# Kernel tuning notes

Measured on AMD Instinct MI355X. Metric: run time of the kernel, lower is better.

Reference implementation:

```python
import jax, jax.numpy as jnp
import numpy as np

D = 512      # model dim
NH = 8       # heads
DH = 64      # dim per head
M = 256      # num landmarks
ITERS = 6    # pinv iterations
EPS = 1e-5   # layernorm eps


def layer_norm(x, g, b):
    mu = x.mean(-1, keepdims=True)
    var = ((x - mu) ** 2).mean(-1, keepdims=True)
    return (x - mu) * jax.lax.rsqrt(var + EPS) * g + b


def moore_penrose_pinv(x, iters=ITERS):
    abs_x = jnp.abs(x)
    col = abs_x.sum(-1)
    row = abs_x.sum(-2)
    z = jnp.swapaxes(x, -1, -2) / (jnp.max(col) * jnp.max(row))
    I = jnp.eye(x.shape[-1], dtype=x.dtype)
    for _ in range(iters):
        xz = x @ z
        z = 0.25 * z @ (13 * I - xz @ (15 * I - xz @ (7 * I - xz)))
    return z


def nystrom_attention(x, w_qkv, w_out, b_out, res_w):
    B, n0, _ = x.shape
    pad = (M - n0 % M) % M
    x = jnp.pad(x, ((0, 0), (pad, 0), (0, 0)))  # pad at front, like lucidrains
    n = n0 + pad
    qkv = x @ w_qkv  # (B, n, 3*D), no bias
    q, k, v = jnp.split(qkv, 3, axis=-1)
    rs = lambda t: t.reshape(B, n, NH, DH).transpose(0, 2, 1, 3)  # (B,H,n,d)
    q = rs(q) * (DH ** -0.5)
    k = rs(k)
    v = rs(v)
    l = n // M
    q_l = q.reshape(B, NH, M, l, DH).mean(3)  # (B,H,M,d) landmark means
    k_l = k.reshape(B, NH, M, l, DH).mean(3)
    s1 = jnp.einsum('bhnd,bhmd->bhnm', q, k_l)
    s2 = jnp.einsum('bhmd,bhld->bhml', q_l, k_l)
    s3 = jnp.einsum('bhmd,bhnd->bhmn', q_l, k)
    a1 = jax.nn.softmax(s1, -1)
    a2 = jax.nn.softmax(s2, -1)
    a3 = jax.nn.softmax(s3, -1)
    out = a1 @ (moore_penrose_pinv(a2) @ (a3 @ v))  # (B,H,n,d)
    # depthwise residual conv over sequence: Conv2d(heads, heads, (33,1), groups=heads)
    res = jax.lax.conv_general_dilated(v, res_w, (1, 1), 'SAME',
                                       feature_group_count=NH,
                                       dimension_numbers=('NCHW', 'OIHW', 'NCHW'))
    out = out + res
    out = out.transpose(0, 2, 1, 3).reshape(B, n, NH * DH) @ w_out + b_out
    return out[:, -n0:]


def dwconv(x, w, b):
    y = jax.lax.conv_general_dilated(x, w, (1, 1), 'SAME',
                                     feature_group_count=x.shape[1],
                                     dimension_numbers=('NCHW', 'OIHW', 'NCHW'))
    return y + b[None, :, None, None]


def ppeg(x, pw7, pb7, pw5, pb5, pw3, pb3, Hh, Ww):
    cls, feat = x[:, :1], x[:, 1:]
    B, _, C = x.shape
    cnn = feat.transpose(0, 2, 1).reshape(B, C, Hh, Ww)
    y = cnn + dwconv(cnn, pw7, pb7) + dwconv(cnn, pw5, pb5) + dwconv(cnn, pw3, pb3)
    y = y.reshape(B, C, Hh * Ww).transpose(0, 2, 1)
    return jnp.concatenate([cls, y], axis=1)


def _forward(x, w_fc1, b_fc1, cls_token, ln1_g, ln1_b, qkv1_w, out1_w, out1_b, res1_w,
             ln2_g, ln2_b, qkv2_w, out2_w, out2_b, res2_w,
             pw7, pb7, pw5, pb5, pw3, pb3, lnf_g, lnf_b, w_fc2, b_fc2):
    h = jax.nn.relu(x @ w_fc1 + b_fc1)  # (B, N, 512)
    Hn = h.shape[1]
    s = int(np.ceil(np.sqrt(Hn)))  # static grid side
    add = s * s - Hn
    h = jnp.concatenate([h, h[:, :add]], axis=1)
    B = h.shape[0]
    cls = jnp.broadcast_to(cls_token, (B, 1, D))
    h = jnp.concatenate([cls, h], axis=1)
    h = h + nystrom_attention(layer_norm(h, ln1_g, ln1_b), qkv1_w, out1_w, out1_b, res1_w)
    h = ppeg(h, pw7, pb7, pw5, pb5, pw3, pb3, s, s)
    h = h + nystrom_attention(layer_norm(h, ln2_g, ln2_b), qkv2_w, out2_w, out2_b, res2_w)
    h = layer_norm(h, lnf_g, lnf_b)[:, 0]
    return h @ w_fc2 + b_fc2


def setup_inputs() -> dict:
    key = jax.random.key(0)
    ks = jax.random.split(key, 16)
    g = lambda k, shp, s=0.02: jax.random.normal(k, shp, dtype=jnp.float32) * s
    z = lambda n: jnp.zeros((n,), jnp.float32)
    o = lambda n: jnp.ones((n,), jnp.float32)
    B, N, DIN, NC = 2, 10000, 1024, 2
    return {
        'x': jax.random.normal(ks[0], (B, N, DIN), dtype=jnp.float32),
        'w_fc1': g(ks[1], (DIN, D)), 'b_fc1': z(D),
        'cls_token': g(ks[2], (1, 1, D), 1.0),
        'ln1_g': o(D), 'ln1_b': z(D),
        'qkv1_w': g(ks[3], (D, 3 * D)),
        'out1_w': g(ks[4], (D, D)), 'out1_b': z(D),
        'res1_w': g(ks[5], (NH, 1, 33, 1)),
        'ln2_g': o(D), 'ln2_b': z(D),
        'qkv2_w': g(ks[6], (D, 3 * D)),
        'out2_w': g(ks[7], (D, D)), 'out2_b': z(D),
        'res2_w': g(ks[8], (NH, 1, 33, 1)),
        'pw7': g(ks[9], (D, 1, 7, 7)), 'pb7': z(D),
        'pw5': g(ks[10], (D, 1, 5, 5)), 'pb5': z(D),
        'pw3': g(ks[11], (D, 1, 3, 3)), 'pb3': z(D),
        'lnf_g': o(D), 'lnf_b': z(D),
        'w_fc2': g(ks[12], (D, NC)), 'b_fc2': z(NC),
    }


def reference(x, w_fc1, b_fc1, cls_token, ln1_g, ln1_b, qkv1_w, out1_w, out1_b, res1_w,
              ln2_g, ln2_b, qkv2_w, out2_w, out2_b, res2_w,
              pw7, pb7, pw5, pb5, pw3, pb3, lnf_g, lnf_b, w_fc2, b_fc2):
    logits = _forward(x, w_fc1, b_fc1, cls_token, ln1_g, ln1_b, qkv1_w, out1_w, out1_b, res1_w,
                      ln2_g, ln2_b, qkv2_w, out2_w, out2_b, res2_w,
                      pw7, pb7, pw5, pb5, pw3, pb3, lnf_g, lnf_b, w_fc2, b_fc2)
    Y_prob = jax.nn.softmax(logits, -1)
    Y_hat = jnp.argmax(logits, -1)
    return logits, Y_prob, Y_hat
```

## Files before the change

### kernel.cpp

```cpp
#include <hip/hip_runtime.h>
#include <math.h>

#define FLAG_RELU 1
#define FLAG_BIAS 2
#define FLAG_ACC  4
#define FLAG_ATOMIC 8

static constexpr int BB   = 2;
static constexpr int N0   = 10000;
static constexpr int DIN  = 1024;
static constexpr int D    = 512;
static constexpr int NH   = 8;
static constexpr int DH   = 64;
static constexpr int MM   = 256;
static constexpr int SEQ  = 10240;
static constexpr int PADR = 239;
static constexpr int NTOK = 10001;
static constexpr int LL   = 40;
static constexpr float EPS_ = 1e-5f;

typedef short short8v __attribute__((ext_vector_type(8)));
typedef float f32x4 __attribute__((ext_vector_type(4)));

__device__ __forceinline__ void atomicMaxPosF(float* addr, float v) {
// ... 83 lines not shown
            size_t gb = (size_t)(n0 + srow) * ldbt + k0 + 32 + scg;
            pb0 = *(const uint4*)(BtH + gb); pb1 = *(const uint4*)(BtH + gb + 8);
            pb2 = *(const uint4*)(BtL + gb); pb3 = *(const uint4*)(BtL + gb + 8);
        }
        short8v ah[4], al[4];
        #pragma unroll
        for (int mi = 0; mi < 4; mi++) {
            int row = wm*64 + mi*16 + r;
            ah[mi] = *(const short8v*)&AsH[q*1024 + row*8];
            al[mi] = *(const short8v*)&AsL[q*1024 + row*8];
        }
        #pragma unroll
        for (int ni = 0; ni < 4; ni++) {
            int col = wn*64 + ni*16 + r;
            short8v bh = *(const short8v*)&BsH[q*1024 + col*8];
            short8v bl = *(const short8v*)&BsL[q*1024 + col*8];
            #pragma unroll
            for (int mi = 0; mi < 4; mi++) {
                acc[mi][ni] = __builtin_amdgcn_mfma_f32_16x16x32_bf16(ah[mi], bh, acc[mi][ni], 0,0,0);
                acc[mi][ni] = __builtin_amdgcn_mfma_f32_16x16x32_bf16(ah[mi], bl, acc[mi][ni], 0,0,0);
                acc[mi][ni] = __builtin_amdgcn_mfma_f32_16x16x32_bf16(al[mi], bh, acc[mi][ni], 0,0,0);
            }
        }
        __syncthreads();
    }
    #pragma unroll
    for (int mi = 0; mi < 4; mi++)
        #pragma unroll
        for (int ni = 0; ni < 4; ni++) {
            int gcol = n0 + wn*64 + ni*16 + r;
            float qs = (gcol < qcols) ? qscale : 1.f;
            float bv = (flags & FLAG_BIAS) ? bias[gcol] : 0.f;
            #pragma unroll
            for (int rg = 0; rg < 4; rg++) {
                int grow = m0 + wm*64 + mi*16 + q*4 + rg;
                if (grow >= M) continue;
                float v = acc[mi][ni][rg] * qs + bv;
                if (flags & FLAG_RELU) v = fmaxf(v, 0.f);
                float* cp = C + (size_t)grow * ldc + gcol;
                if (flags & FLAG_ACC) v += *cp;
                *cp = v;
            }
        }
}

__global__ __launch_bounds__(256)
void mbgemm64(const float* __restrict__ Abase, long long sAb, long long sAh, long long sAz, int lda,
              const ushort* __restrict__ BtH, const ushort* __restrict__ BtL,
              const float* __restrict__ Bnt, long long sBb, long long sBh, int ldb,
              float* __restrict__ Cbase, long long sCb, long long sCh, long long sCz, int ldc,
              ushort* __restrict__ eTH, ushort* __restrict__ eTL, long long sT, int ldct,
              const float* __restrict__ rowM, const float* __restrict__ rowI,
              int M, int N, int K, int nchunk,
              float dg, float bsc, float osc, int slab0, int flags)
{
    __shared__ ushort AsH[4*64*8], AsL[4*64*8], BsH[4*64*8], BsL[4*64*8];
    int zi = blockIdx.z / nchunk, ch = blockIdx.z % nchunk;
    int g = slab0 + zi, b = g >> 3, h = g & 7;
    const float* A = Abase + (size_t)b*sAb + (size_t)h*sAh + (size_t)zi*sAz;
    float* C = Cbase ? (Cbase + (size_t)b*sCb + (size_t)h*sCh + (size_t)zi*sCz) : nullptr;
    int kpc = K / nchunk;
    int kb = ch * kpc, ke = kb + kpc;
    int t = threadIdx.x;
    int m0 = blockIdx.y * 64, n0 = blockIdx.x * 64;
    int w = t >> 6, lane = t & 63, q = lane >> 4, r = lane & 15;
    int wm = w >> 1, wn = w & 1;
    f32x4 acc[2][2];
    #pragma unroll
    for (int i = 0; i < 2; i++)
        #pragma unroll
        for (int j = 0; j < 2; j++) acc[i][j] = (f32x4){0.f,0.f,0.f,0.f};

    int srow = t >> 2, scg = (t & 3) * 8;
    int qg = t & 3;
    float rmv = 0.f, riv = 1.f;
    bool doexp = (rowM != nullptr);
    if (doexp) {
        rmv = rowM[(size_t)zi * MM + m0 + srow];
        riv = rowI[(size_t)zi * MM + m0 + srow];
    }
    const float* Abp = Bnt ? (Bnt + (size_t)b*sBb + (size_t)h*sBh) : nullptr;
    float4 pa0, pa1;
    float4 pf0, pf1;
    uint4  pu0, pu1;
    {
        const float* ap = A + (size_t)(m0 + srow) * lda + kb + scg;
        pa0 = *(const float4*)ap; pa1 = *(const float4*)(ap+4);
        if (Bnt) {
            const float* bp = Abp + (size_t)(n0 + srow) * ldb + kb + scg;
            pf0 = *(const float4*)bp; pf1 = *(const float4*)(bp+4);
        } else {
            size_t gb = (size_t)b*sBb + (size_t)h*sBh + (size_t)(n0 + srow) * ldb + kb + scg;
            pu0 = *(const uint4*)(BtH + gb); pu1 = *(const uint4*)(BtL + gb);
        }
    }
    for (int k0 = kb; k0 < ke; k0 += 32) {
        {
            float4 qa0 = pa0, qa1 = pa1;
            if (doexp) {
                qa0.x = expf(qa0.x - rmv) * riv; qa0.y = expf(qa0.y - rmv) * riv;
                qa0.z = expf(qa0.z - rmv) * riv; qa0.w = expf(qa0.w - rmv) * riv;
                qa1.x = expf(qa1.x - rmv) * riv; qa1.y = expf(qa1.y - rmv) * riv;
                qa1.z = expf(qa1.z - rmv) * riv; qa1.w = expf(qa1.w - rmv) * riv;
            }
            ushort hb[8], lb[8];
            split4(qa0, &hb[0], &lb[0]);
            split4(qa1, &hb[4], &lb[4]);
            *(uint4*)&AsH[qg*512 + srow*8] = *(uint4*)&hb[0];
            *(uint4*)&AsL[qg*512 + srow*8] = *(uint4*)&lb[0];
            if (Bnt) {
                ushort hc[8], lc[8];
                split4(pf0, &hc[0], &lc[0]);
                split4(pf1, &hc[4], &lc[4]);
                *(uint4*)&BsH[qg*512 + srow*8] = *(uint4*)&hc[0];
                *(uint4*)&BsL[qg*512 + srow*8] = *(uint4*)&lc[0];
            } else {
                *(uint4*)&BsH[qg*512 + srow*8] = pu0;
                *(uint4*)&BsL[qg*512 + srow*8] = pu1;
            }
        }
        __syncthreads();
        if (k0 + 32 < ke) {
            const float* ap = A + (size_t)(m0 + srow) * lda + k0 + 32 + scg;
            pa0 = *(const float4*)ap; pa1 = *(const float4*)(ap+4);
            if (Bnt) {
                const float* bp = Abp + (size_t)(n0 + srow) * ldb + k0 + 32 + scg;
                pf0 = *(const float4*)bp; pf1 = *(const float4*)(bp+4);
            } else {
                size_t gb = (size_t)b*sBb + (size_t)h*sBh + (size_t)(n0 + srow) * ldb + k0 + 32 + scg;
                pu0 = *(const uint4*)(BtH + gb); pu1 = *(const uint4*)(BtL + gb);
            }
        }
        short8v ah[2], al[2];
        #pragma unroll
        for (int mi = 0; mi < 2; mi++) {
            int row = wm*32 + mi*16 + r;
            ah[mi] = *(const short8v*)&AsH[q*512 + row*8];
            al[mi] = *(const short8v*)&AsL[q*512 + row*8];
        }
        #pragma unroll
        for (int ni = 0; ni < 2; ni++) {
            int col = wn*32 + ni*16 + r;
            short8v bh = *(const short8v*)&BsH[q*512 + col*8];
            short8v bl = *(const short8v*)&BsL[q*512 + col*8];
            #pragma unroll
            for (int mi = 0; mi < 2; mi++) {
                acc[mi][ni] = __builtin_amdgcn_mfma_f32_16x16x32_bf16(ah[mi], bh, acc[mi][ni], 0,0,0);
                acc[mi][ni] = __builtin_amdgcn_mfma_f32_16x16x32_bf16(ah[mi], bl, acc[mi][ni], 0,0,0);
                acc[mi][ni] = __builtin_amdgcn_mfma_f32_16x16x32_bf16(al[mi], bh, acc[mi][ni], 0,0,0);
            }
        }
        __syncthreads();
    }
    bool dgnz = (dg != 0.f);
    #pragma unroll
    for (int mi = 0; mi < 2; mi++)
        #pragma unroll
        for (int ni = 0; ni < 2; ni++) {
            int gm0 = m0 + wm*32 + mi*16 + q*4;
            int gn  = n0 + wn*32 + ni*16 + r;
            float v[4];
            #pragma unroll
            for (int rg = 0; rg < 4; rg++) {
                float u = bsc * acc[mi][ni][rg];
                if (dgnz) u += dg * A[(size_t)(gm0+rg) * lda + gn];
                v[rg] = osc * u;
            }
            if (C) {
                if (flags & FLAG_ATOMIC) {
                    #pragma unroll
                    for (int rg = 0; rg < 4; rg++)
                        atomicAdd(C + (size_t)(gm0+rg) * ldc + gn, v[rg]);
                } else {
                    #pragma unroll
                    for (int rg = 0; rg < 4; rg++)
                        C[(size_t)(gm0+rg) * ldc + gn] = v[rg];
                }
            }
            if (eTH) {
                ushort4 hv, lv;
                hv.x = f2bf(v[0]); lv.x = f2bf(v[0] - bf2f(hv.x));
                hv.y = f2bf(v[1]); lv.y = f2bf(v[1] - bf2f(hv.y));
                hv.z = f2bf(v[2]); lv.z = f2bf(v[2] - bf2f(hv.z));
                hv.w = f2bf(v[3]); lv.w = f2bf(v[3] - bf2f(hv.w));
                size_t to = (size_t)g * sT + (size_t)gn * ldct + gm0;
                *(ushort4*)(eTH + to) = hv;
                *(ushort4*)(eTL + to) = lv;
            }
        }
}

__global__ __launch_bounds__(256)
void a1_fused(const float* __restrict__ qkv,
              const ushort* __restrict__ klH, const ushort* __restrict__ klL,
              const ushort* __restrict__ wbH, const ushort* __restrict__ wbL,
              float* __restrict__ attn)
{
    constexpr int LP = 264;
    __shared__ ushort PcH[32*LP], PcL[32*LP];
    __shared__ float redm[4][32];
    __shared__ float reds[4][32];
    int g = blockIdx.y, b = g >> 3, h = g & 7;
    int tok0 = blockIdx.x * 32;
    int t = threadIdx.x;
    int w = t >> 6, lane = t & 63, q = lane >> 4, r = lane & 15;

    f32x4 acc[2][4];
    #pragma unroll
    for (int i = 0; i < 2; i++)
        #pragma unroll
        for (int j = 0; j < 4; j++) acc[i][j] = (f32x4){0.f,0.f,0.f,0.f};
    #pragma unroll
    for (int k0 = 0; k0 < 64; k0 += 32) {
        short8v ah[2], al[2];
        #pragma unroll
        for (int mi = 0; mi < 2; mi++) {
            const float* ap = qkv + ((size_t)b*SEQ + tok0 + mi*16 + r) * 1536
                            + h*DH + k0 + q*8;
            split8r(ap, ah[mi], al[mi]);
        }
        #pragma unroll
        for (int ni = 0; ni < 4; ni++) {
            size_t kb = ((size_t)g*MM + w*64 + ni*16 + r) * DH + k0 + q*8;
            short8v bh = *(const short8v*)(klH + kb);
            short8v bl = *(const short8v*)(klL + kb);
            #pragma unroll
            for (int mi = 0; mi < 2; mi++) {
                acc[mi][ni] = __builtin_amdgcn_mfma_f32_16x16x32_bf16(ah[mi], bh, acc[mi][ni], 0,0,0);
                acc[mi][ni] = __builtin_amdgcn_mfma_f32_16x16x32_bf16(ah[mi], bl, acc[mi][ni], 0,0,0);
                acc[mi][ni] = __builtin_amdgcn_mfma_f32_16x16x32_bf16(al[mi], bh, acc[mi][ni], 0,0,0);
            }
        }
    }
    #pragma unroll
    for (int mi = 0; mi < 2; mi++)
        #pragma unroll
        for (int rg = 0; rg < 4; rg++) {
            float m = fmaxf(fmaxf(acc[mi][0][rg], acc[mi][1][rg]),
                            fmaxf(acc[mi][2][rg], acc[mi][3][rg]));
            for (int o = 8; o > 0; o >>= 1) m = fmaxf(m, __shfl_xor(m, o));
            if (r == 0) redm[w][mi*16 + q*4 + rg] = m;
        }
    __syncthreads();
    #pragma unroll
    for (int mi = 0; mi < 2; mi++)
        #pragma unroll
        for (int rg = 0; rg < 4; rg++) {
            int row = mi*16 + q*4 + rg;
            float gm = fmaxf(fmaxf(redm[0][row], redm[1][row]),
                             fmaxf(redm[2][row], redm[3][row]));
            float s = 0.f;
            #pragma unroll
            for (int ni = 0; ni < 4; ni++) {
                float e = expf(acc[mi][ni][rg] - gm);
                acc[mi][ni][rg] = e;
                s += e;
                int col = w*64 + ni*16 + r;
                ushort hv = f2bf(e);
                PcH[row*LP + col] = hv;
                PcL[row*LP + col] = f2bf(e - bf2f(hv));
            }
            for (int o = 8; o > 0; o >>= 1) s += __shfl_xor(s, o);
            if (r == 0) reds[w][row] = s;
        }
    __syncthreads();
    int wm = w & 1, wn = w >> 1;
    int prow = wm*16 + r;
    f32x4 oacc[2];
    #pragma unroll
    for (int ni = 0; ni < 2; ni++) oacc[ni] = (f32x4){0.f,0.f,0.f,0.f};
    #pragma unroll
    for (int k0 = 0; k0 < 8; k0++) {
        short8v ph = *(const short8v*)&PcH[prow*LP + k0*32 + q*8];
        short8v pl = *(const short8v*)&PcL[prow*LP + k0*32 + q*8];
        #pragma unroll
        for (int ni = 0; ni < 2; ni++) {
            size_t wo = ((size_t)g*64 + wn*32 + ni*16 + r) * MM + k0*32 + q*8;
            short8v bh = *(const short8v*)(wbH + wo);
            short8v bl = *(const short8v*)(wbL + wo);
            oacc[ni] = __builtin_amdgcn_mfma_f32_16x16x32_bf16(ph, bh, oacc[ni], 0,0,0);
            oacc[ni] = __builtin_amdgcn_mfma_f32_16x16x32_bf16(ph, bl, oacc[ni], 0,0,0);
            oacc[ni] = __builtin_amdgcn_mfma_f32_16x16x32_bf16(pl, bh, oacc[ni], 0,0,0);
        }
    }
    float inv[4];
    #pragma unroll
    for (int rg = 0; rg < 4; rg++) {
        int row = wm*16 + q*4 + rg;
        inv[rg] = 1.0f / (reds[0][row] + reds[1][row] + reds[2][row] + reds[3][row]);
    }
    #pragma unroll
    for (int ni = 0; ni < 2; ni++)
        #pragma unroll
        for (int rg = 0; rg < 4; rg++) {
            int tok = tok0 + wm*16 + q*4 + rg;
            attn[((size_t)b*SEQ + tok) * D + h*DH + wn*32 + ni*16 + r] = oacc[ni][rg] * inv[rg];
        }
}

__global__ __launch_bounds__(256)
void convsplitT(const float* __restrict__ in, ushort* __restrict__ oh, ushort* __restrict__ ol,
                int R, int C, int ldin, long long sInB, long long sInH, long long sInZ,
                int ldo, long long sOutZ)
{
    __shared__ float tile[32][33];
    int z = blockIdx.z, b = z >> 3, h = z & 7;
    const float* I = in + (size_t)b*sInB + (size_t)h*sInH + (size_t)z*sInZ;
    int p0 = blockIdx.x * 32, c0 = blockIdx.y * 32;
    int tx = threadIdx.x & 31, ty = threadIdx.x >> 5;
    #pragma unroll
    for (int k = 0; k < 4; k++) {
        int rr = p0 + ty + k*8, cc = c0 + tx;
        tile[ty + k*8][tx] = (rr < R && cc < C) ? I[(size_t)rr * ldin + cc] : 0.f;
    }
    __syncthreads();
    #pragma unroll
    for (int k = 0; k < 4; k++) {
        int rr = p0 + tx, cc = c0 + ty + k*8;
        if (rr < R && cc < C) {
            float f = tile[tx][ty + k*8];
            ushort hv = f2bf(f);
            size_t o = (size_t)z * sOutZ + (size_t)cc * ldo + rr;
            oh[o] = hv; ol[o] = f2bf(f - bf2f(hv));
        }
    }
}

__global__ void fill_cls(const float* __restrict__ cls, float* __restrict__ H) {
    H[(size_t)blockIdx.x * NTOK * D + threadIdx.x] = cls[threadIdx.x];
}

__global__ __launch_bounds__(256)
void ln_pad(const float* __restrict__ H, const float* __restrict__ g,
            const float* __restrict__ bt, float* __restrict__ out)
{
    int blk = blockIdx.x;
    int b = blk / SEQ, i = blk % SEQ;
    int t = threadIdx.x;
    float* orow = out + (size_t)blk * D;
    if (i < PADR) { orow[t] = 0.f; orow[t+256] = 0.f; return; }
    const float* x = H + ((size_t)b * NTOK + (i - PADR)) * D;
    float v0 = x[t], v1 = x[t+256];
    __shared__ float w1[4], w2[4];
    float s = v0 + v1;
    for (int o = 32; o > 0; o >>= 1) s += __shfl_xor(s, o);
    if ((t & 63) == 0) w1[t >> 6] = s;
    __syncthreads();
    float mu = (w1[0]+w1[1]+w1[2]+w1[3]) * (1.0f / D);
    float d0 = v0 - mu, d1 = v1 - mu;
    float qq = d0*d0 + d1*d1;
    for (int o = 32; o > 0; o >>= 1) qq += __shfl_xor(qq, o);
    if ((t & 63) == 0) w2[t >> 6] = qq;
    __syncthreads();
    float rs = rsqrtf((w2[0]+w2[1]+w2[2]+w2[3]) * (1.0f / D) + EPS_);
    orow[t]     = d0 * rs * g[t]     + bt[t];
    orow[t+256] = d1 * rs * g[t+256] + bt[t+256];
}

__global__ __launch_bounds__(512)
void landmarks(const float* __restrict__ qkv, float* __restrict__ ql,
               float* __restrict__ klt, ushort* __restrict__ klH, ushort* __restrict__ klL)
{
    int blk = blockIdx.x;
    int b = blk >> 8, m = blk & 255;
    int c = threadIdx.x;
    const float* base = qkv + ((size_t)b * SEQ + (size_t)m * LL) * 1536;
    float sq0=0,sq1=0,sq2=0,sq3=0, sk0=0,sk1=0,sk2=0,sk3=0;
    for (int tt = 0; tt < LL; tt += 4) {
        const float* rr = base + (size_t)tt * 1536;
        sq0 += rr[c];          sk0 += rr[512 + c];
        sq1 += rr[1536 + c];   sk1 += rr[1536 + 512 + c];
        sq2 += rr[3072 + c];   sk2 += rr[3072 + 512 + c];
        sq3 += rr[4608 + c];   sk3 += rr[4608 + 512 + c];
    }
    float sq = (sq0+sq1+sq2+sq3) * (1.0f / LL);
    float sk = (sk0+sk1+sk2+sk3) * (1.0f / LL);
    int h = c >> 6, d = c & 63;
    int slab = b * NH + h;
    ql [((size_t)slab * MM + m) * DH + d] = sq;
    klt[((size_t)slab * DH + d) * MM + m] = sk;
    size_t kidx = ((size_t)slab * MM + m) * DH + d;
    ushort kh = f2bf(sk);
    klH[kidx] = kh; klL[kidx] = f2bf(sk - bf2f(kh));
}

__global__ __launch_bounds__(256)
void s2_softmax(const float* __restrict__ ql, const float* __restrict__ klt,
                float* __restrict__ a2)
{
    int blk = blockIdx.x;
    int m = blk & 255, slab = blk >> 8;
    int j = threadIdx.x;
    __shared__ float q[64];
    __shared__ float red[256];
    if (j < 64) q[j] = ql[((size_t)slab * MM + m) * DH + j];
    __syncthreads();
    const float* kt = klt + (size_t)slab * DH * MM;
    float s = 0.f;
    #pragma unroll 8
    for (int kk = 0; kk < 64; kk++) s = fmaf(q[kk], kt[kk*MM + j], s);
    red[j] = s; __syncthreads();
    for (int o = 128; o > 0; o >>= 1) { if (j < o) red[j] = fmaxf(red[j], red[j+o]); __syncthreads(); }
    float mx = red[0]; __syncthreads();
    float e = expf(s - mx);
    red[j] = e; __syncthreads();
    for (int o = 128; o > 0; o >>= 1) { if (j < o) red[j] += red[j+o]; __syncthreads(); }
    a2[((size_t)slab * MM + m) * MM + j] = e / red[0];
}

__global__ void zero_scr(float* s) { if (threadIdx.x < 2) s[threadIdx.x] = 0.f; }

__global__ __launch_bounds__(256)
void a2_alpha(const float* __restrict__ a2, float* __restrict__ scr)
{
    int slab = blockIdx.x, t = threadIdx.x;
    const float* A = a2 + (size_t)slab * MM * MM;
    float cs = 0.f, rs = 0.f;
    for (int rr = 0; rr < MM; rr++) cs += fabsf(A[(size_t)rr * MM + t]);
    for (int cc = 0; cc < MM; cc++) rs += fabsf(A[(size_t)t * MM + cc]);
    __shared__ float red[256];
    red[t] = rs; __syncthreads();
    for (int o = 128; o > 0; o >>= 1) { if (t < o) red[t] = fmaxf(red[t], red[t+o]); __syncthreads(); }
    float mrs = red[0]; __syncthreads();
    red[t] = cs; __syncthreads();
    for (int o = 128; o > 0; o >>= 1) { if (t < o) red[t] = fmaxf(red[t], red[t+o]); __syncthreads(); }
    float mcs = red[0];
    if (t == 0) { atomicMaxPosF(scr + 0, mrs); atomicMaxPosF(scr + 1, mcs); }
}

__global__ __launch_bounds__(256)
void z_init(const float* __restrict__ a2, const float* __restrict__ scr,
            float* __restrict__ z, ushort* __restrict__ zTh, ushort* __restrict__ zTl)
{
    size_t idx = (size_t)blockIdx.x * 256 + threadIdx.x;
    int slab = (int)(idx >> 16), rr = (int)((idx >> 8) & 255), cc = (int)(idx & 255);
    float inv = 1.0f / (scr[0] * scr[1]);
    z[idx] = a2[((size_t)slab << 16) + (size_t)cc * MM + rr] * inv;
    float tv = a2[idx] * inv;
    ushort th = f2bf(tv);
    zTh[idx] = th; zTl[idx] = f2bf(tv - bf2f(th));
}

__global__ __launch_bounds__(256)
void s3_maxsum(const float* __restrict__ s3, float* __restrict__ rowM,
               float* __restrict__ rowI)
{
    const float* row = s3 + (size_t)blockIdx.x * SEQ;
    int t = threadIdx.x;
    float4 v[10];
    #pragma unroll
    for (int i = 0; i < 10; i++) v[i] = *(const float4*)(row + 4*(i*256 + t));
    float mx = -3.4e38f;
    #pragma unroll
    for (int i = 0; i < 10; i++)
        mx = fmaxf(mx, fmaxf(fmaxf(v[i].x, v[i].y), fmaxf(v[i].z, v[i].w)));
    __shared__ float red[4];
    for (int o = 32; o > 0; o >>= 1) mx = fmaxf(mx, __shfl_xor(mx, o));
    if ((t & 63) == 0) red[t >> 6] = mx;
    __syncthreads();
    mx = fmaxf(fmaxf(red[0], red[1]), fmaxf(red[2], red[3]));
    float sum = 0.f;
    #pragma unroll
    for (int i = 0; i < 10; i++) {
        sum += expf(v[i].x - mx) + expf(v[i].y - mx)
             + expf(v[i].z - mx) + expf(v[i].w - mx);
    }
    __shared__ float red2[4];
    for (int o = 32; o > 0; o >>= 1) sum += __shfl_xor(sum, o);
    if ((t & 63) == 0) red2[t >> 6] = sum;
    __syncthreads();
    if (t == 0) {
        rowM[blockIdx.x] = mx;
        rowI[blockIdx.x] = 1.0f / (red2[0] + red2[1] + red2[2] + red2[3]);
    }
}

__global__ __launch_bounds__(512)
void res_add(const float* __restrict__ qkv, const float* __restrict__ rw,
             float* __restrict__ attn)
{
    int blk = blockIdx.x;
    int b = blk / (SEQ/16), i0 = (blk % (SEQ/16)) * 16;
    int c = threadIdx.x, h = c >> 6;
    __shared__ float w[NH*33];
    if (c < NH*33) w[c] = rw[c];
    __syncthreads();
    float acc[16];
    float* ab = attn + ((size_t)b * SEQ + i0) * D + c;
    #pragma unroll
    for (int rr = 0; rr < 16; rr++) acc[rr] = ab[(size_t)rr * D];
    const float* vb = qkv + (size_t)b * SEQ * 1536 + 2*D + c;
    const float* wh = w + h * 33;
    #pragma unroll 4
    for (int jj = 0; jj < 48; jj++) {
        int j = i0 + jj - 16;
        float val = ((unsigned)j < (unsigned)SEQ) ? vb[(size_t)j * 1536] : 0.f;
        #pragma unroll
        for (int rr = 0; rr < 16; rr++) {
            int ky = jj - rr;
            if (ky >= 0 && ky < 33) acc[rr] = fmaf(val, wh[ky], acc[rr]);
        }
    }
    #pragma unroll
    for (int rr = 0; rr < 16; rr++) ab[(size_t)rr * D] = acc[rr];
}

__global__ __launch_bounds__(256)
void t_fw(const float* __restrict__ H, float* __restrict__ P)
{
    __shared__ float tile[32][33];
    int p0 = blockIdx.x * 32, c0 = blockIdx.y * 32, b = blockIdx.z;
    int tx = threadIdx.x & 31, ty = threadIdx.x >> 5;
    #pragma unroll
    for (int k = 0; k < 4; k++) {
        int pos = p0 + ty + k*8;
        tile[ty + k*8][tx] = (pos < 10000)
            ? H[((size_t)b * NTOK + 1 + pos) * D + c0 + tx] : 0.f;
    }
    __syncthreads();
    #pragma unroll
    for (int k = 0; k < 4; k++) {
        int c = c0 + ty + k*8, pos = p0 + tx;
        if (pos < 10000)
            P[((size_t)b * D + c) * 10000 + pos] = tile[tx][ty + k*8];
    }
}

// ... 148 lines not shown
    const float* res2_w = (const float*)d_in[15];
    const float* pw7 = (const float*)d_in[16];
    const float* pb7 = (const float*)d_in[17];
    const float* pw5 = (const float*)d_in[18];
    const float* pb5 = (const float*)d_in[19];
    const float* pw3 = (const float*)d_in[20];
    const float* pb3 = (const float*)d_in[21];
    const float* lnf_g = (const float*)d_in[22];
    const float* lnf_b = (const float*)d_in[23];
    const float* w_fc2 = (const float*)d_in[24];
    const float* b_fc2 = (const float*)d_in[25];

    float* ws = (float*)d_ws;
    size_t off = 0;
    auto alloc = [&](size_t n) { float* p = ws + off; off += (n + 63) & ~(size_t)63; return p; };
    float* H    = alloc((size_t)BB * NTOK * D);
    float* LN   = alloc((size_t)BB * SEQ * D);
    float* QKV  = alloc((size_t)BB * SEQ * 3 * D);
    float* QL   = alloc((size_t)BB * NH * MM * DH);
    float* KLT  = alloc((size_t)BB * NH * DH * MM);
    float* A2   = alloc((size_t)BB * NH * MM * MM);
    float* ZA   = alloc((size_t)BB * NH * MM * MM);
    float* ZB   = alloc((size_t)BB * NH * MM * MM);
    float* XZ   = alloc((size_t)BB * NH * MM * MM);
    float* A3V  = alloc((size_t)BB * NH * MM * DH);
    float* WB   = alloc((size_t)BB * NH * MM * DH);
    float* S3   = alloc((size_t)8 * MM * SEQ);
    float* SCR  = alloc(64);
    float* ROWM = alloc((size_t)8 * MM);
    float* ROWI = alloc((size_t)8 * MM);
    auto ualloc = [&](size_t n) { ushort* p = (ushort*)(ws + off); off += ((n + 127) / 2) & ~(size_t)63; return p; };
    ushort* WTfcH = ualloc((size_t)512 * 1024);
    ushort* WTfcL = ualloc((size_t)512 * 1024);
    ushort* WTqH  = ualloc((size_t)1536 * 512);
    ushort* WTqL  = ualloc((size_t)1536 * 512);
    ushort* WToH  = ualloc((size_t)512 * 512);
    ushort* WToL  = ualloc((size_t)512 * 512);
    ushort* klBH  = ualloc((size_t)16 * MM * DH);
    ushort* klBL  = ualloc((size_t)16 * MM * DH);
    float*  ATTN = LN;
    ushort* VTH  = (ushort*)LN;
    ushort* VTL  = VTH + (size_t)16 * DH * SEQ;
    ushort* A3VTH = (ushort*)ZB;
    ushort* A3VTL = A3VTH + (size_t)16 * DH * MM;
    ushort* WBTH  = A3VTL + (size_t)16 * DH * MM;
    ushort* WBTL  = WBTH  + (size_t)16 * DH * MM;
    ushort* PT   = (ushort*)S3;
    const size_t PS_ = (size_t)16 * 65536;
    ushort* zTAH = PT;            ushort* zTAL = PT + PS_;
    ushort* zTBH = PT + 2*PS_;    ushort* zTBL = PT + 3*PS_;
    ushort* XZTH = PT + 4*PS_;    ushort* XZTL = PT + 5*PS_;
    ushort* T1TH = PT + 6*PS_;    ushort* T1TL = PT + 7*PS_;
    ushort* T2TH = PT + 8*PS_;    ushort* T2TL = PT + 9*PS_;
    (void)ws_size; (void)in_sizes; (void)n_in; (void)out_size;

    convsplitT<<<dim3(32,16,1), 256, 0, stream>>>(w_fc1, WTfcH, WTfcL, 1024, 512, 512, 0,0,0, 1024, 0);
    mgemm128<<<dim3(4, 79, BB), 256, 0, stream>>>(x, DIN, (long long)N0*DIN,
        WTfcH, WTfcL, 1024, H + D, D, (long long)NTOK*D, b_fc1,
        N0, D, DIN, FLAG_BIAS|FLAG_RELU, 0, 1.f);
    fill_cls<<<BB, D, 0, stream>>>(cls, H);

    auto attention = [&](const float* lg, const float* lb,
                         const float* qw, const float* ow,
                         const float* ob, const float* rw)
    {
        convsplitT<<<dim3(16,48,1), 256, 0, stream>>>(qw, WTqH, WTqL, 512, 1536, 1536, 0,0,0, 512, 0);
        convsplitT<<<dim3(16,16,1), 256, 0, stream>>>(ow, WToH, WToL, 512, 512, 512, 0,0,0, 512, 0);
        ln_pad<<<BB*SEQ, 256, 0, stream>>>(H, lg, lb, LN);
        mgemm128<<<dim3(12, 160, 1), 256, 0, stream>>>(LN, D, 0, WTqH, WTqL, D,
            QKV, 3*D, 0, nullptr, BB*SEQ, 3*D, D, 0, D, 0.125f);
        convsplitT<<<dim3(320, 2, 16), 256, 0, stream>>>(QKV + 2*D, VTH, VTL,
            SEQ, DH, 1536, (long long)SEQ*1536, 64, 0, SEQ, (long long)DH*SEQ);
        landmarks<<<BB*MM, 512, 0, stream>>>(QKV, QL, KLT, klBH, klBL);
        s2_softmax<<<BB*NH*MM, 256, 0, stream>>>(QL, KLT, A2);
        zero_scr<<<1, 64, 0, stream>>>(SCR);
        a2_alpha<<<BB*NH, 256, 0, stream>>>(A2, SCR);
        z_init<<<BB*NH*MM*MM/256, 256, 0, stream>>>(A2, SCR, ZA, zTAH, zTAL);
        float* z = ZA; float* zn = ZB;
        ushort *zTcH = zTAH, *zTcL = zTAL, *zTnH = zTBH, *zTnL = zTBL;
        for (int it = 0; it < 6; it++) {
            dim3 g(4, 4, 16);
            mbgemm64<<<g,256,0,stream>>>(A2, 0,0,65536LL, MM,
                zTcH, zTcL, nullptr, 8LL*65536, 65536LL, MM,
                XZ, 0,0,65536LL, MM, XZTH, XZTL, 65536LL, MM,
                nullptr, nullptr,
                MM, MM, MM, 1, 0.f, 1.f, 1.f, 0, 0);
            mbgemm64<<<g,256,0,stream>>>(XZ, 0,0,65536LL, MM,
                XZTH, XZTL, nullptr, 8LL*65536, 65536LL, MM,
                nullptr, 0,0,0, MM, T1TH, T1TL, 65536LL, MM,
                nullptr, nullptr,
                MM, MM, MM, 1, 7.f, -1.f, 1.f, 0, 0);
            mbgemm64<<<g,256,0,stream>>>(XZ, 0,0,65536LL, MM,
                T1TH, T1TL, nullptr, 8LL*65536, 65536LL, MM,
                nullptr, 0,0,0, MM, T2TH, T2TL, 65536LL, MM,
                nullptr, nullptr,
                MM, MM, MM, 1, 15.f, -1.f, 1.f, 0, 0);
            mbgemm64<<<g,256,0,stream>>>(z, 0,0,65536LL, MM,
                T2TH, T2TL, nullptr, 8LL*65536, 65536LL, MM,
                zn, 0,0,65536LL, MM, zTnH, zTnL, 65536LL, MM,
                nullptr, nullptr,
                MM, MM, MM, 1, 13.f, -1.f, 0.25f, 0, 0);
            float* ts = z; z = zn; zn = ts;
            ushort* uh = zTcH; zTcH = zTnH; zTnH = uh;
            ushort* ul = zTcL; zTcL = zTnL; zTnL = ul;
        }
        for (int grp = 0; grp < 2; grp++) {
            int slab0 = grp * 8;
            mbgemm64<<<dim3(160, 4, 8), 256, 0, stream>>>(QL, 8LL*16384, 16384LL, 0, DH,
                nullptr, nullptr, QKV + D, (long long)SEQ*1536, 64LL, 1536,
                S3, 0,0,(long long)MM*SEQ, SEQ, nullptr, nullptr, 0, 0,
                nullptr, nullptr,
                MM, SEQ, DH, 1, 0.f, 1.f, 1.f, slab0, 0);
            s3_maxsum<<<8*MM, 256, 0, stream>>>(S3, ROWM, ROWI);
            hipMemsetAsync(A3V + (size_t)slab0 * MM * DH, 0,
                           (size_t)8 * MM * DH * sizeof(float), stream);
            mbgemm64<<<dim3(1, 4, 8*16), 256, 0, stream>>>(S3, 0,0,(long long)MM*SEQ, SEQ,
                VTH, VTL, nullptr, 8LL*DH*SEQ, (long long)DH*SEQ, SEQ,
                A3V, 8LL*16384, 16384LL, 0, DH, nullptr, nullptr, 0, 0,
                ROWM, ROWI,
                MM, DH, SEQ, 16, 0.f, 1.f, 1.f, slab0, FLAG_ATOMIC);
        }
        convsplitT<<<dim3(8, 2, 16), 256, 0, stream>>>(A3V, A3VTH, A3VTL,
            MM, DH, DH, 0, 0, 16384LL, MM, 16384LL);
        mbgemm64<<<dim3(1, 4, 16), 256, 0, stream>>>(z, 0,0,65536LL, MM,
            A3VTH, A3VTL, nullptr, 8LL*16384, 16384LL, MM,
            WB, 8LL*16384, 16384LL, 0, DH, WBTH, WBTL, 16384LL, MM,
            nullptr, nullptr,
            MM, DH, MM, 1, 0.f, 1.f, 1.f, 0, 0);
        a1_fused<<<dim3(SEQ/32, 16), 256, 0, stream>>>(QKV, klBH, klBL, WBTH, WBTL, ATTN);
        res_add<<<BB*SEQ/16, 512, 0, stream>>>(QKV, rw, ATTN);
        mgemm128<<<dim3(4, 79, BB), 256, 0, stream>>>(ATTN + (size_t)PADR*D, D, (long long)SEQ*D,
            WToH, WToL, D, H, D, (long long)NTOK*D, ob,
            NTOK, D, D, FLAG_BIAS|FLAG_ACC, 0, 1.f);
    };

    attention(ln1_g, ln1_b, qkv1_w, out1_w, out1_b, res1_w);

    {
        float* Pp = S3;
        float* Qp = S3 + (size_t)BB * D * 10000;
        dim3 tg((10000 + 31)/32, D/32, BB);
        t_fw<<<tg, 256, 0, stream>>>(H, Pp);
        ppeg_conv<<<BB*D, 256, 0, stream>>>(Pp, pw7, pb7, pw5, pb5, pw3, pb3, Qp);
        t_bw<<<tg, 256, 0, stream>>>(Qp, H);
    }

    attention(ln2_g, ln2_b, qkv2_w, out2_w, out2_b, res2_w);

    final_head<<<BB, 512, 0, stream>>>(H, lnf_g, lnf_b, w_fc2, b_fc2, (float*)d_out);
}
```

Baseline: 2.371 ms.

## Halve a1_fused token tile to 16 rows and use fast exp intrinsics

The fused landmark-attention kernel now handles 16 tokens per block instead of 32. This halves its shared memory and accumulator registers, doubles the grid, and adds a launch bounds occupancy hint so more blocks can be resident per CU. Separately, expf is replaced with __expf in the softmax paths (a1, a2, s3 row statistics, and the fused GEMM exp). The cost is that each block reloads the k_l and weight operands for half as many tokens, and __expf is slightly less accurate.

```diff
diff --git a/kernel.cpp b/kernel.cpp
--- a/kernel.cpp
+++ b/kernel.cpp
@@ -205,10 +205,10 @@
         {
             float4 qa0 = pa0, qa1 = pa1;
             if (doexp) {
-                qa0.x = expf(qa0.x - rmv) * riv; qa0.y = expf(qa0.y - rmv) * riv;
-                qa0.z = expf(qa0.z - rmv) * riv; qa0.w = expf(qa0.w - rmv) * riv;
-                qa1.x = expf(qa1.x - rmv) * riv; qa1.y = expf(qa1.y - rmv) * riv;
-                qa1.z = expf(qa1.z - rmv) * riv; qa1.w = expf(qa1.w - rmv) * riv;
+                qa0.x = __expf(qa0.x - rmv) * riv; qa0.y = __expf(qa0.y - rmv) * riv;
+                qa0.z = __expf(qa0.z - rmv) * riv; qa0.w = __expf(qa0.w - rmv) * riv;
+                qa1.x = __expf(qa1.x - rmv) * riv; qa1.y = __expf(qa1.y - rmv) * riv;
+                qa1.z = __expf(qa1.z - rmv) * riv; qa1.w = __expf(qa1.w - rmv) * riv;
             }
             ushort hb[8], lb[8];
             split4(qa0, &hb[0], &lb[0]);
@@ -297,112 +297,88 @@
         }
 }
 
-__global__ __launch_bounds__(256)
+__global__ __launch_bounds__(256, 8)
 void a1_fused(const float* __restrict__ qkv,
               const ushort* __restrict__ klH, const ushort* __restrict__ klL,
               const ushort* __restrict__ wbH, const ushort* __restrict__ wbL,
               float* __restrict__ attn)
 {
     constexpr int LP = 264;
-    __shared__ ushort PcH[32*LP], PcL[32*LP];
-    __shared__ float redm[4][32];
-    __shared__ float reds[4][32];
+    __shared__ ushort PcH[16*LP], PcL[16*LP];
+    __shared__ float redm[4][16];
+    __shared__ float reds[4][16];
     int g = blockIdx.y, b = g >> 3, h = g & 7;
-    int tok0 = blockIdx.x * 32;
+    int tok0 = blockIdx.x * 16;
     int t = threadIdx.x;
     int w = t >> 6, lane = t & 63, q = lane >> 4, r = lane & 15;
 
-    f32x4 acc[2][4];
-    #pragma unroll
-    for (int i = 0; i < 2; i++)
-        #pragma unroll
-        for (int j = 0; j < 4; j++) acc[i][j] = (f32x4){0.f,0.f,0.f,0.f};
+    f32x4 acc[4];
+    #pragma unroll
+    for (int j = 0; j < 4; j++) acc[j] = (f32x4){0.f,0.f,0.f,0.f};
     #pragma unroll
     for (int k0 = 0; k0 < 64; k0 += 32) {
-        short8v ah[2], al[2];
-        #pragma unroll
-        for (int mi = 0; mi < 2; mi++) {
-            const float* ap = qkv + ((size_t)b*SEQ + tok0 + mi*16 + r) * 1536
+        short8v ah, al;
+        {
+            const float* ap = qkv + ((size_t)b*SEQ + tok0 + r) * 1536
                             + h*DH + k0 + q*8;
-            split8r(ap, ah[mi], al[mi]);
+            split8r(ap, ah, al);
         }
         #pragma unroll
         for (int ni = 0; ni < 4; ni++) {
             size_t kb = ((size_t)g*MM + w*64 + ni*16 + r) * DH + k0 + q*8;
             short8v bh = *(const short8v*)(klH + kb);
             short8v bl = *(const short8v*)(klL + kb);
-            #pragma unroll
-            for (int mi = 0; mi < 2; mi++) {
-                acc[mi][ni] = __builtin_amdgcn_mfma_f32_16x16x32_bf16(ah[mi], bh, acc[mi][ni], 0,0,0);
-                acc[mi][ni] = __builtin_amdgcn_mfma_f32_16x16x32_bf16(ah[mi], bl, acc[mi][ni], 0,0,0);
-                acc[mi][ni] = __builtin_amdgcn_mfma_f32_16x16x32_bf16(al[mi], bh, acc[mi][ni], 0,0,0);
-            }
-        }
-    }
-    #pragma unroll
-    for (int mi = 0; mi < 2; mi++)
-        #pragma unroll
-        for (int rg = 0; rg < 4; rg++) {
-            float m = fmaxf(fmaxf(acc[mi][0][rg], acc[mi][1][rg]),
-                            fmaxf(acc[mi][2][rg], acc[mi][3][rg]));
-            for (int o = 8; o > 0; o >>= 1) m = fmaxf(m, __shfl_xor(m, o));
-            if (r == 0) redm[w][mi*16 + q*4 + rg] = m;
-        }
-    __syncthreads();
-    #pragma unroll
-    for (int mi = 0; mi < 2; mi++)
-        #pragma unroll
-        for (int rg = 0; rg < 4; rg++) {
-            int row = mi*16 + q*4 + rg;
-            float gm = fmaxf(fmaxf(redm[0][row], redm[1][row]),
-                             fmaxf(redm[2][row], redm[3][row]));
-            float s = 0.f;
-            #pragma unroll
-            for (int ni = 0; ni < 4; ni++) {
-                float e = expf(acc[mi][ni][rg] - gm);
-                acc[mi][ni][rg] = e;
-                s += e;
-                int col = w*64 + ni*16 + r;
-                ushort hv = f2bf(e);
-                PcH[row*LP + col] = hv;
-                PcL[row*LP + col] = f2bf(e - bf2f(hv));
-            }
-            for (int o = 8; o > 0; o >>= 1) s += __shfl_xor(s, o);
-            if (r == 0) reds[w][row] = s;
-        }
-    __syncthreads();
-    int wm = w & 1, wn = w >> 1;
-    int prow = wm*16 + r;
-    f32x4 oacc[2];
-    #pragma unroll
-    for (int ni = 0; ni < 2; ni++) oacc[ni] = (f32x4){0.f,0.f,0.f,0.f};
+            acc[ni] = __builtin_amdgcn_mfma_f32_16x16x32_bf16(ah, bh, acc[ni], 0,0,0);
+            acc[ni] = __builtin_amdgcn_mfma_f32_16x16x32_bf16(ah, bl, acc[ni], 0,0,0);
+            acc[ni] = __builtin_amdgcn_mfma_f32_16x16x32_bf16(al, bh, acc[ni], 0,0,0);
+        }
+    }
+    #pragma unroll
+    for (int rg = 0; rg < 4; rg++) {
+        float m = fmaxf(fmaxf(acc[0][rg], acc[1][rg]),
+                        fmaxf(acc[2][rg], acc[3][rg]));
+        for (int o = 8; o > 0; o >>= 1) m = fmaxf(m, __shfl_xor(m, o));
+        if (r == 0) redm[w][q*4 + rg] = m;
+    }
+    __syncthreads();
+    #pragma unroll
+    for (int rg = 0; rg < 4; rg++) {
+        int row = q*4 + rg;
+        float gm = fmaxf(fmaxf(redm[0][row], redm[1][row]),
+                         fmaxf(redm[2][row], redm[3][row]));
+        float s = 0.f;
+        #pragma unroll
+        for (int ni = 0; ni < 4; ni++) {
+            float e = __expf(acc[ni][rg] - gm);
+            s += e;
+            int col = w*64 + ni*16 + r;
+            ushort hv = f2bf(e);
+            PcH[row*LP + col] = hv;
+            PcL[row*LP + col] = f2bf(e - bf2f(hv));
+        }
+        for (int o = 8; o > 0; o >>= 1) s += __shfl_xor(s, o);
+        if (r == 0) reds[w][row] = s;
+    }
+    __syncthreads();
+    f32x4 oacc = (f32x4){0.f,0.f,0.f,0.f};
     #pragma unroll
     for (int k0 = 0; k0 < 8; k0++) {
-        short8v ph = *(const short8v*)&PcH[prow*LP + k0*32 + q*8];
-        short8v pl = *(const short8v*)&PcL[prow*LP + k0*32 + q*8];
-        #pragma unroll
-        for (int ni = 0; ni < 2; ni++) {
-            size_t wo = ((size_t)g*64 + wn*32 + ni*16 + r) * MM + k0*32 + q*8;
-            short8v bh = *(const short8v*)(wbH + wo);
-            short8v bl = *(const short8v*)(wbL + wo);
-            oacc[ni] = __builtin_amdgcn_mfma_f32_16x16x32_bf16(ph, bh, oacc[ni], 0,0,0);
-            oacc[ni] = __builtin_amdgcn_mfma_f32_16x16x32_bf16(ph, bl, oacc[ni], 0,0,0);
-            oacc[ni] = __builtin_amdgcn_mfma_f32_16x16x32_bf16(pl, bh, oacc[ni], 0,0,0);
-        }
-    }
-    float inv[4];
+        short8v ph = *(const short8v*)&PcH[r*LP + k0*32 + q*8];
+        short8v pl = *(const short8v*)&PcL[r*LP + k0*32 + q*8];
+        size_t wo = ((size_t)g*64 + w*16 + r) * MM + k0*32 + q*8;
+        short8v bh = *(const short8v*)(wbH + wo);
+        short8v bl = *(const short8v*)(wbL + wo);
+        oacc = __builtin_amdgcn_mfma_f32_16x16x32_bf16(ph, bh, oacc, 0,0,0);
+        oacc = __builtin_amdgcn_mfma_f32_16x16x32_bf16(ph, bl, oacc, 0,0,0);
+        oacc = __builtin_amdgcn_mfma_f32_16x16x32_bf16(pl, bh, oacc, 0,0,0);
+    }
     #pragma unroll
     for (int rg = 0; rg < 4; rg++) {
-        int row = wm*16 + q*4 + rg;
-        inv[rg] = 1.0f / (reds[0][row] + reds[1][row] + reds[2][row] + reds[3][row]);
-    }
-    #pragma unroll
-    for (int ni = 0; ni < 2; ni++)
-        #pragma unroll
-        for (int rg = 0; rg < 4; rg++) {
-            int tok = tok0 + wm*16 + q*4 + rg;
-            attn[((size_t)b*SEQ + tok) * D + h*DH + wn*32 + ni*16 + r] = oacc[ni][rg] * inv[rg];
-        }
+        int row = q*4 + rg;
+        float iv = 1.0f / (reds[0][row] + reds[1][row] + reds[2][row] + reds[3][row]);
+        int tok = tok0 + row;
+        attn[((size_t)b*SEQ + tok) * D + h*DH + w*16 + r] = oacc[rg] * iv;
+    }
 }
 
 __global__ __launch_bounds__(256)
@@ -509,7 +485,7 @@
     red[j] = s; __syncthreads();
     for (int o = 128; o > 0; o >>= 1) { if (j < o) red[j] = fmaxf(red[j], red[j+o]); __syncthreads(); }
     float mx = red[0]; __syncthreads();
-    float e = expf(s - mx);
+    float e = __expf(s - mx);
     red[j] = e; __syncthreads();
     for (int o = 128; o > 0; o >>= 1) { if (j < o) red[j] += red[j+o]; __syncthreads(); }
     a2[((size_t)slab * MM + m) * MM + j] = e / red[0];
@@ -569,8 +545,8 @@
     float sum = 0.f;
     #pragma unroll
     for (int i = 0; i < 10; i++) {
-        sum += expf(v[i].x - mx) + expf(v[i].y - mx)
-             + expf(v[i].z - mx) + expf(v[i].w - mx);
+        sum += __expf(v[i].x - mx) + __expf(v[i].y - mx)
+             + __expf(v[i].z - mx) + __expf(v[i].w - mx);
     }
     __shared__ float red2[4];
     for (int o = 32; o > 0; o >>= 1) sum += __shfl_xor(sum, o);
@@ -909,7 +885,7 @@
             WB, 8LL*16384, 16384LL, 0, DH, WBTH, WBTL, 16384LL, MM,
             nullptr, nullptr,
             MM, DH, MM, 1, 0.f, 1.f, 1.f, 0, 0);
-        a1_fused<<<dim3(SEQ/32, 16), 256, 0, stream>>>(QKV, klBH, klBL, WBTH, WBTL, ATTN);
+        a1_fused<<<dim3(SEQ/16, 16), 256, 0, stream>>>(QKV, klBH, klBL, WBTH, WBTL, ATTN);
         res_add<<<BB*SEQ/16, 512, 0, stream>>>(QKV, rw, ATTN);
         mgemm128<<<dim3(4, 79, BB), 256, 0, stream>>>(ATTN + (size_t)PADR*D, D, (long long)SEQ*D,
             WToH, WToL, D, H, D, (long long)NTOK*D, ob,
```

Result: slower. 2.448 ms (+3.3%).

## Fuse per-tile softmax max/sum into S3 GEMM epilogue and use fast exp

Applied to the files above, without the earlier changes.

The S3 score GEMM now computes per-tile row maxima and exp-sums in its epilogue and writes them to scratch. A small rowcomb kernel merges these partials into the row max and inverse sum, replacing the separate s3_maxsum pass that re-read the whole S3 matrix. Several expf calls in the softmax paths also become __expf for cheaper transcendental evaluation. In exchange the GEMM epilogue gains extra shuffles and two block barriers, and the fast exp slightly reduces accuracy.

```diff
diff --git a/kernel.cpp b/kernel.cpp
--- a/kernel.cpp
+++ b/kernel.cpp
@@ -159,7 +159,8 @@
               ushort* __restrict__ eTH, ushort* __restrict__ eTL, long long sT, int ldct,
               const float* __restrict__ rowM, const float* __restrict__ rowI,
               int M, int N, int K, int nchunk,
-              float dg, float bsc, float osc, int slab0, int flags)
+              float dg, float bsc, float osc, int slab0, int flags,
+              float* __restrict__ tmOut, float* __restrict__ tsOut)
 {
     __shared__ ushort AsH[4*64*8], AsL[4*64*8], BsH[4*64*8], BsL[4*64*8];
     int zi = blockIdx.z / nchunk, ch = blockIdx.z % nchunk;
@@ -205,10 +206,10 @@
         {
             float4 qa0 = pa0, qa1 = pa1;
             if (doexp) {
-                qa0.x = expf(qa0.x - rmv) * riv; qa0.y = expf(qa0.y - rmv) * riv;
-                qa0.z = expf(qa0.z - rmv) * riv; qa0.w = expf(qa0.w - rmv) * riv;
-                qa1.x = expf(qa1.x - rmv) * riv; qa1.y = expf(qa1.y - rmv) * riv;
-                qa1.z = expf(qa1.z - rmv) * riv; qa1.w = expf(qa1.w - rmv) * riv;
+                qa0.x = __expf(qa0.x - rmv) * riv; qa0.y = __expf(qa0.y - rmv) * riv;
+                qa0.z = __expf(qa0.z - rmv) * riv; qa0.w = __expf(qa0.w - rmv) * riv;
+                qa1.x = __expf(qa1.x - rmv) * riv; qa1.y = __expf(qa1.y - rmv) * riv;
+                qa1.z = __expf(qa1.z - rmv) * riv; qa1.w = __expf(qa1.w - rmv) * riv;
             }
             ushort hb[8], lb[8];
             split4(qa0, &hb[0], &lb[0]);
@@ -295,6 +296,67 @@
                 *(ushort4*)(eTL + to) = lv;
             }
         }
+    if (tmOut) {
+        float* smax = (float*)AsH;
+        float* ssum = smax + 128;
+        #pragma unroll
+        for (int mi = 0; mi < 2; mi++)
+            #pragma unroll
+            for (int rg = 0; rg < 4; rg++) {
+                float a0 = osc * (bsc * acc[mi][0][rg]);
+                float a1 = osc * (bsc * acc[mi][1][rg]);
+                float m_ = fmaxf(a0, a1);
+                #pragma unroll
+                for (int o = 8; o > 0; o >>= 1) m_ = fmaxf(m_, __shfl_xor(m_, o));
+                if (r == 0) smax[wn*64 + wm*32 + mi*16 + q*4 + rg] = m_;
+            }
+        __syncthreads();
+        #pragma unroll
+        for (int mi = 0; mi < 2; mi++)
+            #pragma unroll
+            for (int rg = 0; rg < 4; rg++) {
+                int row = wm*32 + mi*16 + q*4 + rg;
+                float cm = fmaxf(smax[row], smax[64 + row]);
+                float a0 = osc * (bsc * acc[mi][0][rg]);
+                float a1 = osc * (bsc * acc[mi][1][rg]);
+                float s_ = __expf(a0 - cm) + __expf(a1 - cm);
+                #pragma unroll
+                for (int o = 8; o > 0; o >>= 1) s_ += __shfl_xor(s_, o);
+                if (r == 0) ssum[wn*64 + row] = s_;
+            }
+        __syncthreads();
+        if (wn == 0 && r == 0) {
+            #pragma unroll
+            for (int mi = 0; mi < 2; mi++)
+                #pragma unroll
+                for (int rg = 0; rg < 4; rg++) {
+                    int row = wm*32 + mi*16 + q*4 + rg;
+                    float cm = fmaxf(smax[row], smax[64 + row]);
+                    size_t o = ((size_t)zi * MM + m0 + row) * (size_t)gridDim.x + blockIdx.x;
+                    tmOut[o] = cm;
+                    tsOut[o] = ssum[row] + ssum[64 + row];
+                }
+        }
+    }
+}
+
+__global__ __launch_bounds__(256)
+void rowcomb(const float* __restrict__ tm, const float* __restrict__ ts,
+             float* __restrict__ rowM, float* __restrict__ rowI, int ntiles)
+{
+    int row = blockIdx.x * 4 + (threadIdx.x >> 6);
+    int lane = threadIdx.x & 63;
+    const float* tmr = tm + (size_t)row * ntiles;
+    const float* tsr = ts + (size_t)row * ntiles;
+    float m = -3.4e38f;
+    for (int i = lane; i < ntiles; i += 64) m = fmaxf(m, tmr[i]);
+    #pragma unroll
+    for (int o = 32; o > 0; o >>= 1) m = fmaxf(m, __shfl_xor(m, o));
+    float s = 0.f;
+    for (int i = lane; i < ntiles; i += 64) s += tsr[i] * __expf(tmr[i] - m);
+    #pragma unroll
+    for (int o = 32; o > 0; o >>= 1) s += __shfl_xor(s, o);
+    if (lane == 0) { rowM[row] = m; rowI[row] = 1.0f / s; }
 }
 
 __global__ __launch_bounds__(256)
@@ -359,7 +421,7 @@
             float s = 0.f;
             #pragma unroll
             for (int ni = 0; ni < 4; ni++) {
-                float e = expf(acc[mi][ni][rg] - gm);
+                float e = __expf(acc[mi][ni][rg] - gm);
                 acc[mi][ni][rg] = e;
                 s += e;
                 int col = w*64 + ni*16 + r;
@@ -509,7 +571,7 @@
     red[j] = s; __syncthreads();
     for (int o = 128; o > 0; o >>= 1) { if (j < o) red[j] = fmaxf(red[j], red[j+o]); __syncthreads(); }
     float mx = red[0]; __syncthreads();
-    float e = expf(s - mx);
+    float e = __expf(s - mx);
     red[j] = e; __syncthreads();
     for (int o = 128; o > 0; o >>= 1) { if (j < o) red[j] += red[j+o]; __syncthreads(); }
     a2[((size_t)slab * MM + m) * MM + j] = e / red[0];
@@ -546,40 +608,6 @@
     float tv = a2[idx] * inv;
     ushort th = f2bf(tv);
     zTh[idx] = th; zTl[idx] = f2bf(tv - bf2f(th));
-}
-
-__global__ __launch_bounds__(256)
-void s3_maxsum(const float* __restrict__ s3, float* __restrict__ rowM,
-               float* __restrict__ rowI)
-{
-    const float* row = s3 + (size_t)blockIdx.x * SEQ;
-    int t = threadIdx.x;
-    float4 v[10];
-    #pragma unroll
-    for (int i = 0; i < 10; i++) v[i] = *(const float4*)(row + 4*(i*256 + t));
-    float mx = -3.4e38f;
-    #pragma unroll
-    for (int i = 0; i < 10; i++)
-        mx = fmaxf(mx, fmaxf(fmaxf(v[i].x, v[i].y), fmaxf(v[i].z, v[i].w)));
-    __shared__ float red[4];
-    for (int o = 32; o > 0; o >>= 1) mx = fmaxf(mx, __shfl_xor(mx, o));
-    if ((t & 63) == 0) red[t >> 6] = mx;
-    __syncthreads();
-    mx = fmaxf(fmaxf(red[0], red[1]), fmaxf(red[2], red[3]));
-    float sum = 0.f;
-    #pragma unroll
-    for (int i = 0; i < 10; i++) {
-        sum += expf(v[i].x - mx) + expf(v[i].y - mx)
-             + expf(v[i].z - mx) + expf(v[i].w - mx);
-    }
-    __shared__ float red2[4];
-    for (int o = 32; o > 0; o >>= 1) sum += __shfl_xor(sum, o);
-    if ((t & 63) == 0) red2[t >> 6] = sum;
-    __syncthreads();
-    if (t == 0) {
-        rowM[blockIdx.x] = mx;
-        rowI[blockIdx.x] = 1.0f / (red2[0] + red2[1] + red2[2] + red2[3]);
-    }
 }
 
 __global__ __launch_bounds__(512)
@@ -834,6 +862,8 @@
     ushort* XZTH = PT + 4*PS_;    ushort* XZTL = PT + 5*PS_;
     ushort* T1TH = PT + 6*PS_;    ushort* T1TL = PT + 7*PS_;
     ushort* T2TH = PT + 8*PS_;    ushort* T2TL = PT + 9*PS_;
+    float* TM = XZ;
+    float* TS = XZ + (size_t)8 * MM * 160;
     (void)ws_size; (void)in_sizes; (void)n_in; (void)out_size;
 
     convsplitT<<<dim3(32,16,1), 256, 0, stream>>>(w_fc1, WTfcH, WTfcL, 1024, 512, 512, 0,0,0, 1024, 0);
@@ -866,22 +896,22 @@
                 zTcH, zTcL, nullptr, 8LL*65536, 65536LL, MM,
                 XZ, 0,0,65536LL, MM, XZTH, XZTL, 65536LL, MM,
                 nullptr, nullptr,
-                MM, MM, MM, 1, 0.f, 1.f, 1.f, 0, 0);
+                MM, MM, MM, 1, 0.f, 1.f, 1.f, 0, 0, nullptr, nullptr);
             mbgemm64<<<g,256,0,stream>>>(XZ, 0,0,65536LL, MM,
                 XZTH, XZTL, nullptr, 8LL*65536, 65536LL, MM,
                 nullptr, 0,0,0, MM, T1TH, T1TL, 65536LL, MM,
                 nullptr, nullptr,
-                MM, MM, MM, 1, 7.f, -1.f, 1.f, 0, 0);
+                MM, MM, MM, 1, 7.f, -1.f, 1.f, 0, 0, nullptr, nullptr);
             mbgemm64<<<g,256,0,stream>>>(XZ, 0,0,65536LL, MM,
                 T1TH, T1TL, nullptr, 8LL*65536, 65536LL, MM,
                 nullptr, 0,0,0, MM, T2TH, T2TL, 65536LL, MM,
                 nullptr, nullptr,
-                MM, MM, MM, 1, 15.f, -1.f, 1.f, 0, 0);
+                MM, MM, MM, 1, 15.f, -1.f, 1.f, 0, 0, nullptr, nullptr);
             mbgemm64<<<g,256,0,stream>>>(z, 0,0,65536LL, MM,
                 T2TH, T2TL, nullptr, 8LL*65536, 65536LL, MM,
                 zn, 0,0,65536LL, MM, zTnH, zTnL, 65536LL, MM,
                 nullptr, nullptr,
-                MM, MM, MM, 1, 13.f, -1.f, 0.25f, 0, 0);
+                MM, MM, MM, 1, 13.f, -1.f, 0.25f, 0, 0, nullptr, nullptr);
             float* ts = z; z = zn; zn = ts;
             ushort* uh = zTcH; zTcH = zTnH; zTnH = uh;
             ushort* ul = zTcL; zTcL = zTnL; zTnL = ul;
@@ -892,15 +922,15 @@
                 nullptr, nullptr, QKV + D, (long long)SEQ*1536, 64LL, 1536,
                 S3, 0,0,(long long)MM*SEQ, SEQ, nullptr, nullptr, 0, 0,
                 nullptr, nullptr,
-                MM, SEQ, DH, 1, 0.f, 1.f, 1.f, slab0, 0);
-            s3_maxsum<<<8*MM, 256, 0, stream>>>(S3, ROWM, ROWI);
+                MM, SEQ, DH, 1, 0.f, 1.f, 1.f, slab0, 0, TM, TS);
+            rowcomb<<<(8*MM)/4, 256, 0, stream>>>(TM, TS, ROWM, ROWI, 160);
             hipMemsetAsync(A3V + (size_t)slab0 * MM * DH, 0,
                            (size_t)8 * MM * DH * sizeof(float), stream);
             mbgemm64<<<dim3(1, 4, 8*16), 256, 0, stream>>>(S3, 0,0,(long long)MM*SEQ, SEQ,
                 VTH, VTL, nullptr, 8LL*DH*SEQ, (long long)DH*SEQ, SEQ,
                 A3V, 8LL*16384, 16384LL, 0, DH, nullptr, nullptr, 0, 0,
                 ROWM, ROWI,
-                MM, DH, SEQ, 16, 0.f, 1.f, 1.f, slab0, FLAG_ATOMIC);
+                MM, DH, SEQ, 16, 0.f, 1.f, 1.f, slab0, FLAG_ATOMIC, nullptr, nullptr);
         }
         convsplitT<<<dim3(8, 2, 16), 256, 0, stream>>>(A3V, A3VTH, A3VTL,
             MM, DH, DH, 0, 0, 16384LL, MM, 16384LL);
@@ -908,7 +938,7 @@
             A3VTH, A3VTL, nullptr, 8LL*16384, 16384LL, MM,
             WB, 8LL*16384, 16384LL, 0, DH, WBTH, WBTL, 16384LL, MM,
             nullptr, nullptr,
-            MM, DH, MM, 1, 0.f, 1.f, 1.f, 0, 0);
+            MM, DH, MM, 1, 0.f, 1.f, 1.f, 0, 0, nullptr, nullptr);
         a1_fused<<<dim3(SEQ/32, 16), 256, 0, stream>>>(QKV, klBH, klBL, WBTH, WBTL, ATTN);
         res_add<<<BB*SEQ/16, 512, 0, stream>>>(QKV, rw, ATTN);
         mgemm128<<<dim3(4, 79, BB), 256, 0, stream>>>(ATTN + (size_t)PADR*D, D, (long long)SEQ*D,
```

Result: slower. 2.456 ms (+3.6%).
